# Kernel optimization log

Hardware: AMD Instinct MI355X
Metric: run time of the kernel (lower is better)

Reference implementation:

```python
import jax, jax.numpy as jnp
import numpy as np

B, D, H, W, K = 64, 256, 32, 32, 512


def setup_inputs() -> dict:
    key = jax.random.key(0)
    k1, k2 = jax.random.split(key)
    x = jax.random.normal(k1, (B, D, H, W), dtype=jnp.float32)
    # module inits codebook with torch.rand (uniform [0,1)), shape (emb_dim, num_emb)
    weight = jax.random.uniform(k2, (D, K), dtype=jnp.float32)
    return {"x": x, "weight": weight}


def reference(x, weight):
    """VQ-VAE nearest-embedding lookup.

    x: (B, D, H, W), weight: (D, K).
    Returns (quantized (B, D, H, W), argmin (B, H, W)).
    """
    b, d, h, w = x.shape
    n = h * w
    xf = x.reshape(b, d, n)                       # (B, D, N)
    x_sq = jnp.sum(xf * xf, axis=1)               # (B, N)
    e_sq = jnp.sum(weight * weight, axis=0)       # (K,)
    cross = jnp.einsum('bdn,dk->bnk', xf, weight)  # (B, N, K) GEMM
    dist = x_sq[:, :, None] - 2.0 * cross + e_sq[None, None, :]
    argmin = jnp.argmin(dist, axis=-1)            # (B, N)
    quant = jnp.take(weight, argmin, axis=1)      # (D, B, N) gather of code vectors
    quant = jnp.transpose(quant, (1, 0, 2)).reshape(b, d, h, w)
    return quant, argmin.reshape(b, h, w)
```

## Files before the change

### kernel.cpp

```cpp
#include <hip/hip_runtime.h>

#define DIM    256
#define KCODE  512
#define NPOS   1024
#define BATCH  64
#define NPB    64
#define KSTEPS 16
#define EPS    0.01f

using f16x8  = __attribute__((ext_vector_type(8))) _Float16;
using f32x16 = __attribute__((ext_vector_type(16))) float;

#define WS_CNT   0
#define WS_ESQ   64
#define WS_WPK   4096
#define WS_WT    (4096 + 524288)
#define WS_LIST  (4096 + 1048576)

__global__ __launch_bounds__(256) void prep(const float* __restrict__ w,
                                            _Float16* __restrict__ wpk,
                                            float* __restrict__ wT,
                                            float* __restrict__ esq,
                                            int* __restrict__ cnt) {
    __shared__ float ts[32][33];
    __shared__ double sh[8][32];
    const int tid = threadIdx.x;
    const int blk = blockIdx.x;
    if (blk < 128) {
        int gidx = blk * 4 + (tid >> 6);
        int dg = gidx & 1, cg = (gidx >> 1) & 15, t = gidx >> 5;
        int lane = tid & 63, L = lane & 31, h5 = lane >> 5;
        f16x8 out;
#pragma unroll
        for (int j = 0; j < 8; ++j) {
            float v = w[(t * 16 + h5 * 8 + j) * KCODE + cg * 32 + L];
            _Float16 h = (_Float16)v;
            out[j] = dg ? (_Float16)(v - (float)h) : h;
        }
        *(f16x8*)(wpk + (size_t)gidx * 512 + lane * 8) = out;
    } else if (blk < 256) {
        int tt = blk - 128;
        int kt = tt >> 3, dt = tt & 7;
        int c = tid & 31, rl = tid >> 5;
#pragma unroll
        for (int r = 0; r < 4; ++r) {
            int dloc = rl * 4 + r;
            ts[dloc][c] = w[(dt * 32 + dloc) * KCODE + kt * 32 + c];
        }
        __syncthreads();
#pragma unroll
        for (int r = 0; r < 4; ++r) {
            int kloc = rl * 4 + r;
            wT[(size_t)(kt * 32 + kloc) * DIM + dt * 32 + c] = ts[c][kloc];
        }
    } else if (blk < 272) {
        int idx = blk - 256;
        int code = idx * 32 + (tid & 31);
        int sl = tid >> 5;
        double s = 0.0;
        for (int d = sl * 32; d < sl * 32 + 32; ++d) {
            double v = (double)w[d * KCODE + code];
            s = fma(v, v, s);
        }
        sh[sl][tid & 31] = s;
        __syncthreads();
        if (tid < 32) {
            double t = 0.0;
            for (int i = 0; i < 8; ++i) t += sh[i][tid];
            esq[idx * 32 + tid] = (float)t;
        }
    } else {
        if (tid == 0) *cnt = 0;
    }
}

__global__ __launch_bounds__(256, 2) void vq_main(
    const float* __restrict__ x, const _Float16* __restrict__ wpk,
    const float* __restrict__ esq, const float* __restrict__ wT,
    float* __restrict__ quant, float* __restrict__ argm,
    int* __restrict__ cnt, int* __restrict__ list) {

    __shared__ __align__(128) unsigned char smem[67584];
    unsigned char* Bt = smem;
    float* esq_s  = (float*)(smem + 65536);
    float* red1   = (float*)smem;
    float* red2   = (float*)(smem + 1024);
    int*   redi   = (int*)(smem + 2048);
    float* qt     = (float*)(smem + 3072);
    float* bestv  = (float*)(smem + 19712);
    int*   idxbuf = (int*)(smem + 19968);

    const int tid  = threadIdx.x;
    const int wv   = tid >> 6;
    const int lane = tid & 63;
    const int L    = lane & 31;
    const int h5   = lane >> 5;

    const int p0 = blockIdx.x * NPB;
    const int b  = p0 >> 10;
    const int n0 = p0 & (NPOS - 1);

    const int pos = tid & 63;
    const int tg  = tid >> 6;

    esq_s[tid] = esq[tid];
    esq_s[tid + 256] = esq[tid + 256];

#pragma unroll
    for (int tt = 0; tt < 4; ++tt) {
        int t = tg * 4 + tt;
#pragma unroll
        for (int hh = 0; hh < 2; ++hh) {
            const float* xp = x + ((size_t)b * DIM + t * 16 + hh * 8) * NPOS + n0 + pos;
            f16x8 vh, vl;
#pragma unroll
            for (int j = 0; j < 8; ++j) {
                float v = xp[(size_t)j * NPOS];
                _Float16 h = (_Float16)v;
                vh[j] = h;
                vl[j] = (_Float16)(v - (float)h);
            }
            *(f16x8*)(Bt + ((((t * 2 + hh) * 2) + 0) * NPB + pos) * 16) = vh;
            *(f16x8*)(Bt + ((((t * 2 + hh) * 2) + 1) * NPB + pos) * 16) = vl;
        }
    }
    __syncthreads();

    f32x16 acc[4][2] = {};

#pragma unroll
    for (int t = 0; t < KSTEPS; ++t) {
        const unsigned char* abase =
            (const unsigned char*)wpk + (size_t)(t * 32 + wv * 8) * 1024 + lane * 16;
        f16x8 Ah[4][2];
#pragma unroll
        for (int fm = 0; fm < 4; ++fm)
#pragma unroll
            for (int dg = 0; dg < 2; ++dg)
                Ah[fm][dg] = *(const f16x8*)(abase + (fm * 2 + dg) * 1024);
        f16x8 Bf[2][2];
#pragma unroll
        for (int fn = 0; fn < 2; ++fn)
#pragma unroll
            for (int dg = 0; dg < 2; ++dg)
                Bf[fn][dg] = *(const f16x8*)(
                    Bt + ((((t * 2 + h5) * 2) + dg) * NPB + fn * 32 + L) * 16);
        __builtin_amdgcn_s_setprio(1);
#pragma unroll
        for (int fm = 0; fm < 4; ++fm)
#pragma unroll
            for (int fn = 0; fn < 2; ++fn)
                acc[fm][fn] = __builtin_amdgcn_mfma_f32_32x32x16_f16(Ah[fm][0], Bf[fn][0], acc[fm][fn], 0, 0, 0);
#pragma unroll
        for (int fm = 0; fm < 4; ++fm)
#pragma unroll
            for (int fn = 0; fn < 2; ++fn)
                acc[fm][fn] = __builtin_amdgcn_mfma_f32_32x32x16_f16(Ah[fm][1], Bf[fn][0], acc[fm][fn], 0, 0, 0);
#pragma unroll
        for (int fm = 0; fm < 4; ++fm)
#pragma unroll
            for (int fn = 0; fn < 2; ++fn)
                acc[fm][fn] = __builtin_amdgcn_mfma_f32_32x32x16_f16(Ah[fm][0], Bf[fn][1], acc[fm][fn], 0, 0, 0);
        __builtin_amdgcn_s_setprio(0);
    }
    __syncthreads();

    float v1[2] = {3.4e38f, 3.4e38f};
    float v2[2] = {3.4e38f, 3.4e38f};
#pragma unroll
    for (int fm = 0; fm < 4; ++fm)
#pragma unroll
        for (int r = 0; r < 16; ++r) {
            int code = wv * 128 + fm * 32 + (r & 3) + 8 * (r >> 2) + 4 * h5;
            float e = esq_s[code];
#pragma unroll
            for (int fn = 0; fn < 2; ++fn) {
                float s = fmaf(-2.f, acc[fm][fn][r], e);
                acc[fm][fn][r] = s;
                float lo_ = fminf(s, v1[fn]);
                float hi_ = fmaxf(s, v1[fn]);
                v1[fn] = lo_;
                v2[fn] = fminf(v2[fn], hi_);
            }
        }
#pragma unroll
    for (int fn = 0; fn < 2; ++fn) {
        float o1 = __shfl_xor(v1[fn], 32, 64);
        float o2 = __shfl_xor(v2[fn], 32, 64);
        float mn = fminf(v1[fn], o1);
        float mx = fmaxf(v1[fn], o1);
        v1[fn] = mn;
        v2[fn] = fminf(fminf(v2[fn], o2), mx);
        if (h5 == 0) { red1[wv * NPB + fn * 32 + L] = v1[fn]; red2[wv * NPB + fn * 32 + L] = v2[fn]; }
    }
    __syncthreads();
    if (tid < NPB) {
        float g1 = red1[tid], g2 = red2[tid];
#pragma unroll
        for (int wvi = 1; wvi < 4; ++wvi) {
            float a1 = red1[wvi * NPB + tid], a2 = red2[wvi * NPB + tid];
            float mn = fminf(g1, a1), mx = fmaxf(g1, a1);
            g1 = mn; g2 = fminf(fminf(g2, a2), mx);
        }
        bestv[tid] = g1;
        if (g2 - g1 < EPS) {
            int slot = atomicAdd(cnt, 1);
            list[slot] = p0 + tid;
        }
    }
    __syncthreads();
#pragma unroll
    for (int fn = 0; fn < 2; ++fn) {
        float tgt = bestv[fn * 32 + L];
        int cand = 0x7FFFFFFF;
#pragma unroll
        for (int fm = 0; fm < 4; ++fm)
#pragma unroll
            for (int r = 0; r < 16; ++r) {
                int code = wv * 128 + fm * 32 + (r & 3) + 8 * (r >> 2) + 4 * h5;
                if (acc[fm][fn][r] == tgt) cand = min(cand, code);
            }
        int oc = __shfl_xor(cand, 32, 64);
        cand = min(cand, oc);
        if (h5 == 0) redi[wv * NPB + fn * 32 + L] = cand;
    }
    __syncthreads();
    if (tid < NPB) {
        int bi = redi[tid];
#pragma unroll
        for (int wvi = 1; wvi < 4; ++wvi) bi = min(bi, redi[wvi * NPB + tid]);
        idxbuf[tid] = bi;
        argm[(size_t)b * NPOS + n0 + tid] = (float)bi;
    }
    __syncthreads();

    for (int ch = 0; ch < 4; ++ch) {
#pragma unroll
        for (int it = 0; it < 16; ++it) {
            int pp = it * 4 + wv;
            int bi = idxbuf[pp];
            qt[pp * 65 + lane] = wT[(size_t)bi * DIM + ch * 64 + lane];
        }
        __syncthreads();
#pragma unroll
        for (int i = 0; i < 16; ++i) {
            int d = ch * 64 + i * 4 + tg;
            quant[((size_t)b * DIM + d) * NPOS + n0 + pos] = qt[pos * 65 + i * 4 + tg];
        }
        __syncthreads();
    }
}

__global__ __launch_bounds__(512) void refine(const float* __restrict__ x,
                                              const float* __restrict__ w,
                                              float* __restrict__ quant,
                                              float* __restrict__ argm,
                                              const int* __restrict__ cnt,
                                              const int* __restrict__ list) {
    __shared__ float  xs[DIM];
    __shared__ double dv[512];
    __shared__ int    di[512];
    const int tid = threadIdx.x;
    const int n = *cnt;
    for (int i = blockIdx.x; i < n; i += gridDim.x) {
        const int p = list[i];
        const size_t pb = (size_t)(p >> 10), pn = (size_t)(p & (NPOS - 1));
        if (tid < DIM) xs[tid] = x[(pb * DIM + tid) * NPOS + pn];
        __syncthreads();
        double acc = 0.0, sw = 0.0;
#pragma unroll 8
        for (int d = 0; d < DIM; ++d) {
            double wv = (double)w[d * KCODE + tid];
            double xv = (double)xs[d];
            acc = fma(wv, xv, acc);
            sw  = fma(wv, wv, sw);
        }
        dv[tid] = sw - 2.0 * acc;
        di[tid] = tid;
        __syncthreads();
        for (int off = 256; off > 0; off >>= 1) {
            if (tid < off) {
                double ov = dv[tid + off]; int oi = di[tid + off];
                if (ov < dv[tid] || (ov == dv[tid] && oi < di[tid])) { dv[tid] = ov; di[tid] = oi; }
            }
            __syncthreads();
        }
        const int bsel = di[0];
        if (tid == 0) argm[pb * NPOS + pn] = (float)bsel;
        if (tid < DIM) quant[(pb * DIM + tid) * NPOS + pn] = w[tid * KCODE + bsel];
        __syncthreads();
    }
}

extern "C" void kernel_launch(void* const* d_in, const int* in_sizes, int n_in,
                              void* d_out, int out_size, void* d_ws, size_t ws_size,
                              hipStream_t stream) {
    (void)in_sizes; (void)n_in; (void)out_size; (void)ws_size;
    const float* x = (const float*)d_in[0];
    const float* w = (const float*)d_in[1];
    float* quant = (float*)d_out;
    float* argm  = quant + (size_t)BATCH * DIM * NPOS;
    char* ws = (char*)d_ws;
    int*      cnt = (int*)(ws + WS_CNT);
    float*    esq = (float*)(ws + WS_ESQ);
    _Float16* wpk = (_Float16*)(ws + WS_WPK);
    float*    wT  = (float*)(ws + WS_WT);
    int*      list = (int*)(ws + WS_LIST);

    prep<<<273, 256, 0, stream>>>(w, wpk, wT, esq, cnt);
    vq_main<<<(BATCH * NPOS) / NPB, 256, 0, stream>>>(x, wpk, esq, wT, quant, argm, cnt, list);
    refine<<<2048, 512, 0, stream>>>(x, w, quant, argm, cnt, list);
}
```

Measured before the change: 100.8 us.

## Split vq_main work across 8 waves by codes and positions

Doubles the block size of vq_main from 256 to 512 threads. Each block now has 8 waves that split the 64 positions into two halves and the 512 codes into four quarters, so each wave holds half the accumulators it held before. The intent is more waves per CU to hide latency in the MFMA loop and in the gather and store phases. In exchange, each A fragment loaded from global memory now feeds fewer MFMAs, the setprio hints are dropped, and the launch bound of 4 blocks of 512 threads may not fit given the 67 KB of shared memory per block.

```diff
diff --git a/kernel.cpp b/kernel.cpp
--- a/kernel.cpp
+++ b/kernel.cpp
@@ -74,7 +74,7 @@
     }
 }
 
-__global__ __launch_bounds__(256, 2) void vq_main(
+__global__ __launch_bounds__(512, 4) void vq_main(
     const float* __restrict__ x, const _Float16* __restrict__ wpk,
     const float* __restrict__ esq, const float* __restrict__ wT,
     float* __restrict__ quant, float* __restrict__ argm,
@@ -92,6 +92,8 @@
 
     const int tid  = threadIdx.x;
     const int wv   = tid >> 6;
+    const int wc   = wv & 3;
+    const int wp   = wv >> 2;
     const int lane = tid & 63;
     const int L    = lane & 31;
     const int h5   = lane >> 5;
@@ -104,11 +106,10 @@
     const int tg  = tid >> 6;
 
     esq_s[tid] = esq[tid];
-    esq_s[tid + 256] = esq[tid + 256];
-
-#pragma unroll
-    for (int tt = 0; tt < 4; ++tt) {
-        int t = tg * 4 + tt;
+
+#pragma unroll
+    for (int tt = 0; tt < 2; ++tt) {
+        int t = tg * 2 + tt;
 #pragma unroll
         for (int hh = 0; hh < 2; ++hh) {
             const float* xp = x + ((size_t)b * DIM + t * 16 + hh * 8) * NPOS + n0 + pos;
@@ -126,79 +127,64 @@
     }
     __syncthreads();
 
-    f32x16 acc[4][2] = {};
+    f32x16 acc[4] = {};
 
 #pragma unroll
     for (int t = 0; t < KSTEPS; ++t) {
         const unsigned char* abase =
-            (const unsigned char*)wpk + (size_t)(t * 32 + wv * 8) * 1024 + lane * 16;
+            (const unsigned char*)wpk + (size_t)((t * 16 + wc * 4) * 2) * 1024 + lane * 16;
         f16x8 Ah[4][2];
 #pragma unroll
         for (int fm = 0; fm < 4; ++fm)
 #pragma unroll
             for (int dg = 0; dg < 2; ++dg)
                 Ah[fm][dg] = *(const f16x8*)(abase + (fm * 2 + dg) * 1024);
-        f16x8 Bf[2][2];
-#pragma unroll
-        for (int fn = 0; fn < 2; ++fn)
-#pragma unroll
-            for (int dg = 0; dg < 2; ++dg)
-                Bf[fn][dg] = *(const f16x8*)(
-                    Bt + ((((t * 2 + h5) * 2) + dg) * NPB + fn * 32 + L) * 16);
-        __builtin_amdgcn_s_setprio(1);
-#pragma unroll
-        for (int fm = 0; fm < 4; ++fm)
-#pragma unroll
-            for (int fn = 0; fn < 2; ++fn)
-                acc[fm][fn] = __builtin_amdgcn_mfma_f32_32x32x16_f16(Ah[fm][0], Bf[fn][0], acc[fm][fn], 0, 0, 0);
-#pragma unroll
-        for (int fm = 0; fm < 4; ++fm)
-#pragma unroll
-            for (int fn = 0; fn < 2; ++fn)
-                acc[fm][fn] = __builtin_amdgcn_mfma_f32_32x32x16_f16(Ah[fm][1], Bf[fn][0], acc[fm][fn], 0, 0, 0);
-#pragma unroll
-        for (int fm = 0; fm < 4; ++fm)
-#pragma unroll
-            for (int fn = 0; fn < 2; ++fn)
-                acc[fm][fn] = __builtin_amdgcn_mfma_f32_32x32x16_f16(Ah[fm][0], Bf[fn][1], acc[fm][fn], 0, 0, 0);
-        __builtin_amdgcn_s_setprio(0);
-    }
-    __syncthreads();
-
-    float v1[2] = {3.4e38f, 3.4e38f};
-    float v2[2] = {3.4e38f, 3.4e38f};
+        f16x8 Bf[2];
+#pragma unroll
+        for (int dg = 0; dg < 2; ++dg)
+            Bf[dg] = *(const f16x8*)(
+                Bt + ((((t * 2 + h5) * 2) + dg) * NPB + wp * 32 + L) * 16);
+#pragma unroll
+        for (int fm = 0; fm < 4; ++fm)
+            acc[fm] = __builtin_amdgcn_mfma_f32_32x32x16_f16(Ah[fm][0], Bf[0], acc[fm], 0, 0, 0);
+#pragma unroll
+        for (int fm = 0; fm < 4; ++fm)
+            acc[fm] = __builtin_amdgcn_mfma_f32_32x32x16_f16(Ah[fm][1], Bf[0], acc[fm], 0, 0, 0);
+#pragma unroll
+        for (int fm = 0; fm < 4; ++fm)
+            acc[fm] = __builtin_amdgcn_mfma_f32_32x32x16_f16(Ah[fm][0], Bf[1], acc[fm], 0, 0, 0);
+    }
+    __syncthreads();
+
+    float v1 = 3.4e38f, v2 = 3.4e38f;
 #pragma unroll
     for (int fm = 0; fm < 4; ++fm)
 #pragma unroll
         for (int r = 0; r < 16; ++r) {
-            int code = wv * 128 + fm * 32 + (r & 3) + 8 * (r >> 2) + 4 * h5;
+            int code = wc * 128 + fm * 32 + (r & 3) + 8 * (r >> 2) + 4 * h5;
             float e = esq_s[code];
-#pragma unroll
-            for (int fn = 0; fn < 2; ++fn) {
-                float s = fmaf(-2.f, acc[fm][fn][r], e);
-                acc[fm][fn][r] = s;
-                float lo_ = fminf(s, v1[fn]);
-                float hi_ = fmaxf(s, v1[fn]);
-                v1[fn] = lo_;
-                v2[fn] = fminf(v2[fn], hi_);
-            }
-        }
-#pragma unroll
-    for (int fn = 0; fn < 2; ++fn) {
-        float o1 = __shfl_xor(v1[fn], 32, 64);
-        float o2 = __shfl_xor(v2[fn], 32, 64);
-        float mn = fminf(v1[fn], o1);
-        float mx = fmaxf(v1[fn], o1);
-        v1[fn] = mn;
-        v2[fn] = fminf(fminf(v2[fn], o2), mx);
-        if (h5 == 0) { red1[wv * NPB + fn * 32 + L] = v1[fn]; red2[wv * NPB + fn * 32 + L] = v2[fn]; }
+            float s = fmaf(-2.f, acc[fm][r], e);
+            acc[fm][r] = s;
+            float lo_ = fminf(s, v1);
+            float hi_ = fmaxf(s, v1);
+            v1 = lo_;
+            v2 = fminf(v2, hi_);
+        }
+    {
+        float o1 = __shfl_xor(v1, 32, 64);
+        float o2 = __shfl_xor(v2, 32, 64);
+        float mn = fminf(v1, o1);
+        float mx = fmaxf(v1, o1);
+        v1 = mn;
+        v2 = fminf(fminf(v2, o2), mx);
+        if (h5 == 0) { red1[wc * 64 + wp * 32 + L] = v1; red2[wc * 64 + wp * 32 + L] = v2; }
     }
     __syncthreads();
     if (tid < NPB) {
         float g1 = red1[tid], g2 = red2[tid];
 #pragma unroll
-        for (int wvi = 1; wvi < 4; ++wvi) {
-            float a1 = red1[wvi * NPB + tid], a2 = red2[wvi * NPB + tid];
+        for (int wci = 1; wci < 4; ++wci) {
+            float a1 = red1[wci * 64 + tid], a2 = red2[wci * 64 + tid];
             float mn = fminf(g1, a1), mx = fmaxf(g1, a1);
             g1 = mn; g2 = fminf(fminf(g2, a2), mx);
         }
@@ -209,26 +195,25 @@
         }
     }
     __syncthreads();
-#pragma unroll
-    for (int fn = 0; fn < 2; ++fn) {
-        float tgt = bestv[fn * 32 + L];
+    {
+        float tgt = bestv[wp * 32 + L];
         int cand = 0x7FFFFFFF;
 #pragma unroll
         for (int fm = 0; fm < 4; ++fm)
 #pragma unroll
             for (int r = 0; r < 16; ++r) {
-                int code = wv * 128 + fm * 32 + (r & 3) + 8 * (r >> 2) + 4 * h5;
-                if (acc[fm][fn][r] == tgt) cand = min(cand, code);
+                int code = wc * 128 + fm * 32 + (r & 3) + 8 * (r >> 2) + 4 * h5;
+                if (acc[fm][r] == tgt) cand = min(cand, code);
             }
         int oc = __shfl_xor(cand, 32, 64);
         cand = min(cand, oc);
-        if (h5 == 0) redi[wv * NPB + fn * 32 + L] = cand;
+        if (h5 == 0) redi[wc * 64 + wp * 32 + L] = cand;
     }
     __syncthreads();
     if (tid < NPB) {
         int bi = redi[tid];
 #pragma unroll
-        for (int wvi = 1; wvi < 4; ++wvi) bi = min(bi, redi[wvi * NPB + tid]);
+        for (int wci = 1; wci < 4; ++wci) bi = min(bi, redi[wci * 64 + tid]);
         idxbuf[tid] = bi;
         argm[(size_t)b * NPOS + n0 + tid] = (float)bi;
     }
@@ -236,16 +221,16 @@
 
     for (int ch = 0; ch < 4; ++ch) {
 #pragma unroll
-        for (int it = 0; it < 16; ++it) {
-            int pp = it * 4 + wv;
+        for (int it = 0; it < 8; ++it) {
+            int pp = it * 8 + wv;
             int bi = idxbuf[pp];
             qt[pp * 65 + lane] = wT[(size_t)bi * DIM + ch * 64 + lane];
         }
         __syncthreads();
 #pragma unroll
-        for (int i = 0; i < 16; ++i) {
-            int d = ch * 64 + i * 4 + tg;
-            quant[((size_t)b * DIM + d) * NPOS + n0 + pos] = qt[pos * 65 + i * 4 + tg];
+        for (int i = 0; i < 8; ++i) {
+            int d = ch * 64 + i * 8 + tg;
+            quant[((size_t)b * DIM + d) * NPOS + n0 + pos] = qt[pos * 65 + i * 8 + tg];
         }
         __syncthreads();
     }
@@ -308,6 +293,6 @@
     int*      list = (int*)(ws + WS_LIST);
 
     prep<<<273, 256, 0, stream>>>(w, wpk, wT, esq, cnt);
-    vq_main<<<(BATCH * NPOS) / NPB, 256, 0, stream>>>(x, wpk, esq, wT, quant, argm, cnt, list);
+    vq_main<<<(BATCH * NPOS) / NPB, 512, 0, stream>>>(x, wpk, esq, wT, quant, argm, cnt, list);
     refine<<<2048, 512, 0, stream>>>(x, w, quant, argm, cnt, list);
 }
```

Result: slower. 107.6 us (+6.7%).
